# Optimization experiments

Measured on AMD Instinct MI355X. Metric: run time of the kernel, lower is better.

Reference implementation:

```python
import jax, jax.numpy as jnp
import numpy as np

EMB = 1024
H = 16
DH = 64


def setup_inputs() -> dict:
    key = jax.random.key(0)
    ks = jax.random.split(key, 9)
    s = 1.0 / np.sqrt(EMB)
    so = 1.0 / np.sqrt(H * DH)
    return {
        "x": jax.random.normal(ks[0], (4, 2048, EMB), dtype=jnp.float32),
        "Wq": jax.random.uniform(ks[1], (H * DH, EMB), jnp.float32, -s, s),
        "bq": jax.random.uniform(ks[2], (H * DH,), jnp.float32, -s, s),
        "Wk": jax.random.uniform(ks[3], (H * DH, EMB), jnp.float32, -s, s),
        "bk": jax.random.uniform(ks[4], (H * DH,), jnp.float32, -s, s),
        "Wv": jax.random.uniform(ks[5], (H * DH, EMB), jnp.float32, -s, s),
        "bv": jax.random.uniform(ks[6], (H * DH,), jnp.float32, -s, s),
        "Wo": jax.random.uniform(ks[7], (EMB, H * DH), jnp.float32, -so, so),
        "bo": jax.random.uniform(ks[8], (EMB,), jnp.float32, -so, so),
    }


def reference(x, Wq, bq, Wk, bk, Wv, bv, Wo, bo):
    B, S, E = x.shape
    # project and split heads: [B, H, S, Dh]
    def proj(W, b):
        return (jnp.einsum('bse,de->bsd', x, W) + b).reshape(B, S, H, DH).transpose(0, 2, 1, 3)
    q = proj(Wq, bq)
    k = proj(Wk, bk)
    v = proj(Wv, bv)
    scores = jnp.einsum('bhsd,bhtd->bhst', q / jnp.sqrt(jnp.float32(DH)), k)
    attn = jax.nn.softmax(scores, axis=-1)
    out = jnp.einsum('bhst,bhtd->bhsd', attn, v)  # [B,H,S,Dh]
    out = out.transpose(0, 2, 1, 3).reshape(B, S, H * DH)
    return jnp.einsum('bsd,ed->bse', out, Wo) + bo
```

## Files before the change

kernel.cpp:

```cpp
#include <hip/hip_runtime.h>
#include <hip/hip_bf16.h>
#include <stdint.h>

typedef __bf16 bf16x8 __attribute__((ext_vector_type(8)));
typedef float f32x4 __attribute__((ext_vector_type(4)));
typedef float f32x16 __attribute__((ext_vector_type(16)));
typedef uint32_t u32x4 __attribute__((ext_vector_type(4)));

__device__ __forceinline__ ushort f2bf(float f) {
  uint32_t u = __builtin_bit_cast(uint32_t, f);
  u += 0x7FFFu + ((u >> 16) & 1u);
  return (ushort)(u >> 16);
}

__device__ __forceinline__ uint32_t cvtpk(float lo, float hi) {
  uint32_t r;
  asm("v_cvt_pk_bf16_f32 %0, %1, %2" : "=v"(r) : "v"(lo), "v"(hi));
  return r;
}

__device__ __forceinline__ void p32swap(uint32_t& x, uint32_t& y) {
  asm("v_permlane32_swap_b32 %0, %1" : "+v"(x), "+v"(y));
}

__device__ __forceinline__ void gload16(const void* g, void* l) {
  auto gp = reinterpret_cast<const __attribute__((address_space(1))) char*>(
      reinterpret_cast<uintptr_t>(g));
  auto lp = reinterpret_cast<__attribute__((address_space(3))) char*>(
      reinterpret_cast<uintptr_t>(l));
  __builtin_amdgcn_global_load_lds(gp, lp, 16, 0, 0);
}

__device__ __forceinline__ f32x4 mfma16(bf16x8 a, bf16x8 b, f32x4 c) {
  return __builtin_amdgcn_mfma_f32_16x16x32_bf16(a, b, c, 0, 0, 0);
}
__device__ __forceinline__ f32x16 mfma32(bf16x8 a, bf16x8 b, f32x16 c) {
  return __builtin_amdgcn_mfma_f32_32x32x16_bf16(a, b, c, 0, 0, 0);
}

#define VMW(n) do { asm volatile("s_waitcnt vmcnt(" #n ")" ::: "memory"); \
                    __builtin_amdgcn_sched_barrier(0); } while (0)
#define SBAR __builtin_amdgcn_s_barrier()
#define SCHED0 __builtin_amdgcn_sched_barrier(0)

__global__ void cast_kernel(const float* __restrict__ src, ushort* __restrict__ dst) {
  int i = (blockIdx.x * 256 + threadIdx.x) * 4;
  float4 v = *(const float4*)(src + i);
  ushort4 o;
  o.x = f2bf(v.x); o.y = f2bf(v.y); o.z = f2bf(v.z); o.w = f2bf(v.w);
  *(ushort4*)(dst + i) = o;
}

template <int MODE>
__global__ __launch_bounds__(512, 2) void gemm_k(
    const ushort* __restrict__ A, const ushort* __restrict__ W,
    const float* __restrict__ b0, const float* __restrict__ b1,
    const float* __restrict__ b2,
    ushort* __restrict__ qo, ushort* __restrict__ ko, ushort* __restrict__ vo,
    float* __restrict__ fo)
{
  __shared__ ushort As[3][128 * 64];
  __shared__ ushort Bs[3][256 * 64];
  const int tid = threadIdx.x;
  const int lane = tid & 63, wid = tid >> 6;
  const int wr = wid >> 2, wc = wid & 3;
  const int l15 = lane & 15, l4 = lane >> 4;

  const int wg = blockIdx.x, nwg = gridDim.x, qch = nwg >> 3;
  const int lid = (wg & 7) * qch + (wg >> 3);
  const int bx = lid >> 6, by = lid & 63;
  const int m0 = by * 128, n0 = bx * 256;

  const char* Ag = (const char*)(A + (size_t)m0 * 1024);
  const char* Wg = (const char*)(W + (size_t)n0 * 1024);

  f32x4 acc[4][4] = {};

  const int soff = tid * 16;

  auto STAGE = [&](int d, int kt) {
    const int k0b = kt * 128;
#pragma unroll
    for (int s = 0; s < 2; ++s) {
      int off = soff + s * 8192;
      int row = off >> 7, cb = off & 127;
      int sc = cb ^ ((row & 7) << 4);
      gload16(Ag + (size_t)row * 2048 + k0b + sc, (char*)As[d] + off);
    }
#pragma unroll
    for (int s = 0; s < 4; ++s) {
      int off = soff + s * 8192;
      int row = off >> 7, cb = off & 127;
      int sc = cb ^ ((row & 7) << 4);
      gload16(Wg + (size_t)row * 2048 + k0b + sc, (char*)Bs[d] + off);
    }
  };

  bf16x8 af[4][2], bfr[4][2];

  auto EXTRACT = [&](int d) {
#pragma unroll
    for (int mt = 0; mt < 4; ++mt) {
      int row = wr * 64 + mt * 16 + l15;
      int sw = (row & 7) << 4;
#pragma unroll
      for (int kk = 0; kk < 2; ++kk)
        af[mt][kk] = *(const bf16x8*)((const char*)As[d] + row * 128 +
                                      ((kk * 64 + l4 * 16) ^ sw));
    }
#pragma unroll
    for (int nt = 0; nt < 4; ++nt) {
      int row = wc * 64 + nt * 16 + l15;
      int sw = (row & 7) << 4;
#pragma unroll
      for (int kk = 0; kk < 2; ++kk)
        bfr[nt][kk] = *(const bf16x8*)((const char*)Bs[d] + row * 128 +
                                       ((kk * 64 + l4 * 16) ^ sw));
    }
  };

  auto MFMAS = [&]() {
    __builtin_amdgcn_s_setprio(1);
#pragma unroll
    for (int kk = 0; kk < 2; ++kk)
#pragma unroll
      for (int mt = 0; mt < 4; ++mt)
#pragma unroll
        for (int nt = 0; nt < 4; ++nt)
          acc[mt][nt] = mfma16(af[mt][kk], bfr[nt][kk], acc[mt][nt]);
    __builtin_amdgcn_s_setprio(0);
  };

  STAGE(0, 0);
  STAGE(1, 1);
  VMW(6); SBAR; SCHED0;

#pragma unroll
  for (int t = 0; t < 14; ++t) {
    STAGE((t + 2) % 3, t + 2);
    EXTRACT(t % 3);
    MFMAS();
    VMW(6);
    SBAR; SCHED0;
  }
  EXTRACT(2); MFMAS(); VMW(0); SBAR; SCHED0;
  EXTRACT(0); MFMAS();

  if (MODE == 0) {
    const int seg = n0 >> 10;
    const int nb = n0 & 1023;
    const float* bptr = (seg == 0) ? b0 : (seg == 1) ? b1 : b2;
#pragma unroll
    for (int nt = 0; nt < 4; ++nt) {
      int nl = nb + wc * 64 + nt * 16 + l15;
      int h = nl >> 6, dd = nl & 63;
      float bias = bptr[nl];
#pragma unroll
      for (int mt = 0; mt < 4; ++mt) {
        int m = m0 + wr * 64 + mt * 16 + l4 * 4;
        int b = m >> 11, s = m & 2047;
        if (seg == 2) {
          ushort4 pk;
          pk.x = f2bf(acc[mt][nt][0] + bias);
          pk.y = f2bf(acc[mt][nt][1] + bias);
          pk.z = f2bf(acc[mt][nt][2] + bias);
          pk.w = f2bf(acc[mt][nt][3] + bias);
          *(ushort4*)(vo + (size_t)((b * 16 + h) * 64 + dd) * 2048 + s) = pk;
        } else {
          ushort* dst = (seg == 0) ? qo : ko;
          float sc = (seg == 0) ? 0.18033688011112042f : 1.0f;
#pragma unroll
          for (int r = 0; r < 4; ++r)
            dst[(size_t)((b * 16 + h) * 2048 + s + r) * 64 + dd] =
                f2bf((acc[mt][nt][r] + bias) * sc);
        }
      }
    }
  } else {
#pragma unroll
    for (int nt = 0; nt < 4; ++nt) {
      int n = n0 + wc * 64 + nt * 16 + l15;
      float bias = b0[n];
#pragma unroll
      for (int mt = 0; mt < 4; ++mt) {
        int m = m0 + wr * 64 + mt * 16 + l4 * 4;
#pragma unroll
        for (int r = 0; r < 4; ++r)
          fo[(size_t)(m + r) * 1024 + n] = acc[mt][nt][r] + bias;
      }
    }
  }
}

__global__ __launch_bounds__(256, 2) void attn_k(
    const ushort* __restrict__ Q, const ushort* __restrict__ K,
    const ushort* __restrict__ V, ushort* __restrict__ O)
{
  __shared__ ushort KVs[2][8192];
  const int tid = threadIdx.x, lane = tid & 63;
  const int l31 = lane & 31, hi = lane >> 5;
  const int w = tid >> 6;
  const int bh = blockIdx.x;
  const int b = bh >> 4, h = bh & 15;
  const int q0 = blockIdx.y * 256 + w * 64;
  const ushort* Qh = Q + (size_t)bh * 131072;
  const ushort* Kh = K + (size_t)bh * 131072;
  const ushort* Vh = V + (size_t)bh * 131072;

  bf16x8 qf[2][4];
#pragma unroll
  for (int g = 0; g < 2; ++g)
#pragma unroll
    for (int c = 0; c < 4; ++c)
      qf[g][c] = *(const bf16x8*)(Qh + (size_t)(q0 + g * 32 + l31) * 64 + c * 16 + hi * 8);

  u32x4 onebits;
  onebits[0] = 0x3F803F80u; onebits[1] = 0x3F803F80u;
  onebits[2] = 0x3F803F80u; onebits[3] = 0x3F803F80u;
  const bf16x8 ones = __builtin_bit_cast(bf16x8, onebits);

  f32x16 oacc[2][2] = {};
  float lrun[2] = {0.f, 0.f};

  const int sw = (l31 & 7) << 4;
  const int loff = tid * 16;
  const int srow = loff >> 7, scolb = loff & 127;

  auto STAGE = [&](int buf, int j) {
    char* base = (char*)KVs[buf];
#pragma unroll
    for (int sh = 0; sh < 2; ++sh) {
      int row = srow + sh * 32;
      int off = loff + sh * 4096;
      int sc = scolb ^ ((row & 7) << 4);
      gload16((const char*)Kh + (size_t)j * 8192 + row * 128 + sc, base + off);
      gload16((const char*)Vh + (size_t)row * 4096 + j * 128 + sc, base + 8192 + off);
    }
  };

  STAGE(0, 0);
  __syncthreads();
  int cur = 0;

  for (int j = 0; j < 32; ++j) {
    if (j < 31) STAGE(cur ^ 1, j + 1);
    const char* Kb = (const char*)KVs[cur];
    const char* Vb = Kb + 8192;

    f32x16 sacc[2][2] = {};
    __builtin_amdgcn_s_setprio(1);
#pragma unroll
    for (int t = 0; t < 2; ++t)
#pragma unroll
      for (int c = 0; c < 4; ++c) {
        bf16x8 kfr = *(const bf16x8*)(Kb + (t * 32 + l31) * 128 +
                                      ((c * 32 + hi * 16) ^ sw));
        sacc[0][t] = mfma32(kfr, qf[0][c], sacc[0][t]);
        sacc[1][t] = mfma32(kfr, qf[1][c], sacc[1][t]);
      }
    __builtin_amdgcn_s_setprio(0);

    bf16x8 pb[2][4];
#pragma unroll
    for (int g = 0; g < 2; ++g) {
#pragma unroll
      for (int t = 0; t < 2; ++t)
#pragma unroll
        for (int r = 0; r < 16; ++r)
          sacc[g][t][r] = __builtin_amdgcn_exp2f(sacc[g][t][r]);

      uint32_t wlo[2][4], whi[2][4];
#pragma unroll
      for (int t = 0; t < 2; ++t)
#pragma unroll
        for (int gg = 0; gg < 4; ++gg) {
          wlo[t][gg] = cvtpk(sacc[g][t][gg * 4 + 0], sacc[g][t][gg * 4 + 1]);
          whi[t][gg] = cvtpk(sacc[g][t][gg * 4 + 2], sacc[g][t][gg * 4 + 3]);
        }
#pragma unroll
      for (int c = 0; c < 4; ++c) {
        const int t = c >> 1, gb = (c & 1) * 2;
        uint32_t x0 = wlo[t][gb], y0 = wlo[t][gb + 1];
        p32swap(x0, y0);
        uint32_t x1 = whi[t][gb], y1 = whi[t][gb + 1];
        p32swap(x1, y1);
        u32x4 wv_;
        wv_[0] = x0; wv_[1] = x1; wv_[2] = y0; wv_[3] = y1;
        pb[g][c] = __builtin_bit_cast(bf16x8, wv_);
      }
    }

    f32x16 ssacc[2] = {};
    __builtin_amdgcn_s_setprio(1);
#pragma unroll
    for (int dt = 0; dt < 2; ++dt)
#pragma unroll
      for (int c = 0; c < 4; ++c) {
        bf16x8 vfr = *(const bf16x8*)(Vb + (dt * 32 + l31) * 128 +
                                      ((c * 32 + hi * 16) ^ sw));
        oacc[0][dt] = mfma32(vfr, pb[0][c], oacc[0][dt]);
        oacc[1][dt] = mfma32(vfr, pb[1][c], oacc[1][dt]);
      }
#pragma unroll
    for (int c = 0; c < 4; ++c) {
      ssacc[0] = mfma32(ones, pb[0][c], ssacc[0]);
      ssacc[1] = mfma32(ones, pb[1][c], ssacc[1]);
    }
    __builtin_amdgcn_s_setprio(0);
    lrun[0] += ssacc[0][0];
    lrun[1] += ssacc[1][0];

    __syncthreads();
    cur ^= 1;
  }

#pragma unroll
  for (int g = 0; g < 2; ++g) {
    float linv = 1.0f / lrun[g];
    ushort* Ob = O + (size_t)(b * 2048 + q0 + g * 32 + l31) * 1024 + h * 64;
#pragma unroll
    for (int dt = 0; dt < 2; ++dt)
#pragma unroll
      for (int gg = 0; gg < 4; ++gg) {
        ushort4 o4;
        o4.x = f2bf(oacc[g][dt][gg * 4 + 0] * linv);
        o4.y = f2bf(oacc[g][dt][gg * 4 + 1] * linv);
        o4.z = f2bf(oacc[g][dt][gg * 4 + 2] * linv);
        o4.w = f2bf(oacc[g][dt][gg * 4 + 3] * linv);
        *(ushort4*)(Ob + dt * 32 + gg * 8 + hi * 4) = o4;
      }
  }
}

extern "C" void kernel_launch(void* const* d_in, const int* in_sizes, int n_in,
                              void* d_out, int out_size, void* d_ws, size_t ws_size,
                              hipStream_t stream)
{
  const float* x  = (const float*)d_in[0];
  const float* Wq = (const float*)d_in[1];
  const float* bq = (const float*)d_in[2];
  const float* Wk = (const float*)d_in[3];
  const float* bk = (const float*)d_in[4];
  const float* Wv = (const float*)d_in[5];
  const float* bv = (const float*)d_in[6];
  const float* Wo = (const float*)d_in[7];
  const float* bo = (const float*)d_in[8];
  float* out = (float*)d_out;
  ushort* ws = (ushort*)d_ws;

  ushort* xb   = ws;
  ushort* wqkv = ws + 8388608;
  ushort* wo   = ws + 11534336;
  ushort* qb   = ws + 12582912;
  ushort* kb   = ws + 20971520;
  ushort* vb   = ws + 29360128;

  cast_kernel<<<8192, 256, 0, stream>>>(x, xb);
  cast_kernel<<<1024, 256, 0, stream>>>(Wq, wqkv);
  cast_kernel<<<1024, 256, 0, stream>>>(Wk, wqkv + 1048576);
  cast_kernel<<<1024, 256, 0, stream>>>(Wv, wqkv + 2097152);
  cast_kernel<<<1024, 256, 0, stream>>>(Wo, wo);

  gemm_k<0><<<768, 512, 0, stream>>>(xb, wqkv, bq, bk, bv, qb, kb, vb, nullptr);
  attn_k<<<dim3(64, 8), 256, 0, stream>>>(qb, kb, vb, xb);
  gemm_k<1><<<256, 512, 0, stream>>>(xb, wo, bo, bo, bo, nullptr, nullptr, nullptr, out);
}
```

Measured before the change: 173.3 us.

## Split QKV projection into transposed Q/K GEMM and separate V GEMM

The fused QKV projection is split into two launches. Q and K are computed as W·xᵀ, so accumulator rows map to the head dimension and each lane can write four contiguous bf16 values with a vectorized store, replacing scattered scalar 2-byte stores. V keeps the original orientation and its existing packed transposed store. This trades one larger launch for two smaller ones (512 + 256 blocks), which may reduce wave fill and adds launch overhead.

Result: no change. 173.8 us (+0.3%).

```diff
diff --git a/kernel.cpp b/kernel.cpp
--- a/kernel.cpp
+++ b/kernel.cpp
@@ -53,9 +53,8 @@
 
 template <int MODE>
 __global__ __launch_bounds__(512, 2) void gemm_k(
-    const ushort* __restrict__ A, const ushort* __restrict__ W,
+    const ushort* __restrict__ A, const ushort* __restrict__ Bm,
     const float* __restrict__ b0, const float* __restrict__ b1,
-    const float* __restrict__ b2,
     ushort* __restrict__ qo, ushort* __restrict__ ko, ushort* __restrict__ vo,
     float* __restrict__ fo)
 {
@@ -68,11 +67,12 @@
 
   const int wg = blockIdx.x, nwg = gridDim.x, qch = nwg >> 3;
   const int lid = (wg & 7) * qch + (wg >> 3);
-  const int bx = lid >> 6, by = lid & 63;
+  const int bx = (MODE == 2) ? (lid >> 4) : (lid >> 6);
+  const int by = (MODE == 2) ? (lid & 15) : (lid & 63);
   const int m0 = by * 128, n0 = bx * 256;
 
   const char* Ag = (const char*)(A + (size_t)m0 * 1024);
-  const char* Wg = (const char*)(W + (size_t)n0 * 1024);
+  const char* Wg = (const char*)(Bm + (size_t)n0 * 1024);
 
   f32x4 acc[4][4] = {};
 
@@ -146,34 +146,45 @@
   EXTRACT(2); MFMAS(); VMW(0); SBAR; SCHED0;
   EXTRACT(0); MFMAS();
 
-  if (MODE == 0) {
-    const int seg = n0 >> 10;
-    const int nb = n0 & 1023;
-    const float* bptr = (seg == 0) ? b0 : (seg == 1) ? b1 : b2;
+  if (MODE == 2) {
+    const int seg = m0 >> 10;
+    ushort* dst = seg ? ko : qo;
+    const float* bptr = seg ? b1 : b0;
+    const float sc = seg ? 1.0f : 0.18033688011112042f;
+#pragma unroll
+    for (int mt = 0; mt < 4; ++mt) {
+      int mrow = m0 + wr * 64 + mt * 16 + l4 * 4;
+      int nl = mrow & 1023;
+      int h = nl >> 6, d0 = nl & 63;
+      float4 bias = *(const float4*)(bptr + nl);
+#pragma unroll
+      for (int nt = 0; nt < 4; ++nt) {
+        int s = n0 + wc * 64 + nt * 16 + l15;
+        int b = s >> 11, sl = s & 2047;
+        ushort4 pk;
+        pk.x = f2bf((acc[mt][nt][0] + bias.x) * sc);
+        pk.y = f2bf((acc[mt][nt][1] + bias.y) * sc);
+        pk.z = f2bf((acc[mt][nt][2] + bias.z) * sc);
+        pk.w = f2bf((acc[mt][nt][3] + bias.w) * sc);
+        *(ushort4*)(dst + (size_t)((b * 16 + h) * 2048 + sl) * 64 + d0) = pk;
+      }
+    }
+  } else if (MODE == 0) {
 #pragma unroll
     for (int nt = 0; nt < 4; ++nt) {
-      int nl = nb + wc * 64 + nt * 16 + l15;
+      int nl = n0 + wc * 64 + nt * 16 + l15;
       int h = nl >> 6, dd = nl & 63;
-      float bias = bptr[nl];
+      float bias = b0[nl];
 #pragma unroll
       for (int mt = 0; mt < 4; ++mt) {
         int m = m0 + wr * 64 + mt * 16 + l4 * 4;
         int b = m >> 11, s = m & 2047;
-        if (seg == 2) {
-          ushort4 pk;
-          pk.x = f2bf(acc[mt][nt][0] + bias);
-          pk.y = f2bf(acc[mt][nt][1] + bias);
-          pk.z = f2bf(acc[mt][nt][2] + bias);
-          pk.w = f2bf(acc[mt][nt][3] + bias);
-          *(ushort4*)(vo + (size_t)((b * 16 + h) * 64 + dd) * 2048 + s) = pk;
-        } else {
-          ushort* dst = (seg == 0) ? qo : ko;
-          float sc = (seg == 0) ? 0.18033688011112042f : 1.0f;
-#pragma unroll
-          for (int r = 0; r < 4; ++r)
-            dst[(size_t)((b * 16 + h) * 2048 + s + r) * 64 + dd] =
-                f2bf((acc[mt][nt][r] + bias) * sc);
-        }
+        ushort4 pk;
+        pk.x = f2bf(acc[mt][nt][0] + bias);
+        pk.y = f2bf(acc[mt][nt][1] + bias);
+        pk.z = f2bf(acc[mt][nt][2] + bias);
+        pk.w = f2bf(acc[mt][nt][3] + bias);
+        *(ushort4*)(vo + (size_t)((b * 16 + h) * 64 + dd) * 2048 + s) = pk;
       }
     }
   } else {
@@ -361,7 +372,9 @@
   cast_kernel<<<1024, 256, 0, stream>>>(Wv, wqkv + 2097152);
   cast_kernel<<<1024, 256, 0, stream>>>(Wo, wo);
 
-  gemm_k<0><<<768, 512, 0, stream>>>(xb, wqkv, bq, bk, bv, qb, kb, vb, nullptr);
+  gemm_k<2><<<512, 512, 0, stream>>>(wqkv, xb, bq, bk, qb, kb, nullptr, nullptr);
+  gemm_k<0><<<256, 512, 0, stream>>>(xb, wqkv + 2097152, bv, nullptr,
+                                     nullptr, nullptr, vb, nullptr);
   attn_k<<<dim3(64, 8), 256, 0, stream>>>(qb, kb, vb, xb);
-  gemm_k<1><<<256, 512, 0, stream>>>(xb, wo, bo, bo, bo, nullptr, nullptr, nullptr, out);
-}
+  gemm_k<1><<<256, 512, 0, stream>>>(xb, wo, bo, nullptr, nullptr, nullptr, nullptr, out);
+}
```
